# Kernel optimization log

Hardware: AMD Instinct MI355X
Metric: run time of the kernel (lower is better)

Reference implementation:

```python
import jax, jax.numpy as jnp
from jax import lax
import numpy as np

NUM_Q, DIM_S, SIZE_M = 13523, 128, 64
B, T = 64, 200

def setup_inputs() -> dict:
    key = jax.random.key(0)
    ks = jax.random.split(key, 16)
    def kn(k, shape, fan_in):
        # kaiming_normal_ (fan_in, relu gain sqrt(2))
        return jax.random.normal(k, shape, jnp.float32) * np.sqrt(2.0 / fan_in)
    return {
        "q": jax.random.randint(ks[0], (B, T), 0, NUM_Q),
        "r": jax.random.randint(ks[1], (B, T), 0, 2),
        "k_emb": jax.random.normal(ks[2], (NUM_Q, DIM_S), jnp.float32),
        "v_emb": jax.random.normal(ks[3], (2 * NUM_Q, DIM_S), jnp.float32),
        "Mk": kn(ks[4], (SIZE_M, DIM_S), DIM_S),
        "Mv0": kn(ks[5], (SIZE_M, DIM_S), DIM_S),
        "f_W": jax.random.normal(ks[6], (DIM_S, 2 * DIM_S), jnp.float32) / np.sqrt(2 * DIM_S),
        "f_b": jnp.zeros((DIM_S,), jnp.float32),
        "p_W": jax.random.normal(ks[7], (1, DIM_S), jnp.float32) / np.sqrt(DIM_S),
        "p_b": jnp.zeros((1,), jnp.float32),
        "e_W": jax.random.normal(ks[8], (DIM_S, DIM_S), jnp.float32) / np.sqrt(DIM_S),
        "e_b": jnp.zeros((DIM_S,), jnp.float32),
        "a_W": jax.random.normal(ks[9], (DIM_S, DIM_S), jnp.float32) / np.sqrt(DIM_S),
        "a_b": jnp.zeros((DIM_S,), jnp.float32),
    }

def reference(q, r, k_emb, v_emb, Mk, Mv0, f_W, f_b, p_W, p_b, e_W, e_b, a_W, a_b):
    num_q = k_emb.shape[0]
    x = q + num_q * r                       # [B,T]
    k = k_emb[q]                            # [B,T,D]
    v = v_emb[x]                            # [B,T,D]
    w = jax.nn.softmax(jnp.einsum('btd,md->btm', k, Mk), axis=-1)  # [B,T,M]
    e = jax.nn.sigmoid(v @ e_W.T + e_b)     # [B,T,D]
    a = jnp.tanh(v @ a_W.T + a_b)           # [B,T,D]
    batch = q.shape[0]
    Mv_init = jnp.broadcast_to(Mv0, (batch,) + Mv0.shape)  # [B,M,D]

    def step(Mvt, inp):
        wt, et, at = inp  # [B,M],[B,D],[B,D]
        we = wt[:, :, None]  # [B,M,1]
        Mvt = Mvt * (1.0 - we * et[:, None, :]) + we * at[:, None, :]
        return Mvt, Mvt

    _, Mv_seq = lax.scan(step, Mv_init,
                         (w.transpose(1, 0, 2), e.transpose(1, 0, 2), a.transpose(1, 0, 2)))
    # Mv: [B, T+1, M, D], index t holds memory BEFORE write at step t
    Mv = jnp.concatenate([Mv_init[None], Mv_seq], axis=0).transpose(1, 0, 2, 3)
    read = jnp.einsum('btm,btmd->btd', w, Mv[:, :-1])  # read pre-update memory
    f = jnp.tanh(jnp.concatenate([read, k], axis=-1) @ f_W.T + f_b)
    p = jax.nn.sigmoid(f @ p_W.T + p_b).squeeze(-1)    # [B,T]
    return p, Mv
```

## Files before the change

### kernel.cpp

```cpp
#include <hip/hip_runtime.h>
#include <cstdint>
#include <cstddef>

#define B_   64
#define T_   200
#define NQ_  13523
#define NTOK (B_*T_)

#define O_MKT  0
#define O_EWT  8192
#define O_AWT  24576
#define O_FWT  40960
#define O_W    73728
#define O_EV   892928
#define O_AV   2531328
#define O_KF   4169728
#define O_PART 5808128

#define TOKA 32
#define LSTR 36

typedef float f4v __attribute__((ext_vector_type(4)));

__device__ __forceinline__ float sigmoidf_(float x){
  return __fdividef(1.f, 1.f + __expf(-x));
}
__device__ __forceinline__ float tanhf_(float x){
  float ax = fabsf(x);
  float e  = __expf(-2.f*ax);
  float t  = __fdividef(1.f - e, 1.f + e);
  return copysignf(t, x);
}

__device__ __forceinline__ void nt_store4(const float4& v, float* p){
  f4v t; t.x = v.x; t.y = v.y; t.z = v.z; t.w = v.w;
  __builtin_nontemporal_store(t, (f4v*)p);
}

__global__ __launch_bounds__(256) void k_prep(const float* __restrict__ Mk,
    const float* __restrict__ eW, const float* __restrict__ aW,
    const float* __restrict__ fW, float* __restrict__ ws)
{
  int i = blockIdx.x*256 + threadIdx.x;
  if (i < 8192){  int j = i>>6, m = i&63;  ws[O_MKT+i] = Mk[m*128 + j]; }
  if (i < 16384){ int j = i>>7, d = i&127; ws[O_EWT+i] = eW[d*128 + j];
                                           ws[O_AWT+i] = aW[d*128 + j]; }
  if (i < 32768){ int c = i>>7, d = i&127; ws[O_FWT+i] = fW[d*256 + c]; }
}

__global__ __launch_bounds__(256) void k_embed(const int* __restrict__ q,
    const int* __restrict__ r, const float* __restrict__ kE,
    const float* __restrict__ vE, const float* __restrict__ eb,
    const float* __restrict__ ab, float* __restrict__ ws)
{
  __shared__ float Kt[128*LSTR];
  __shared__ float Vt[128*LSTR];
  __shared__ int qx[2*TOKA];
  const int tid = threadIdx.x;
  const int it0 = blockIdx.x * TOKA;

  if (tid < TOKA){
    int qq = q[it0+tid];
    qx[tid]      = qq;
    qx[TOKA+tid] = qq + NQ_*r[it0+tid];
  }
  __syncthreads();

  {
    const int j  = tid & 127;
    const int wg = tid >> 7;
    #pragma unroll
    for (int rr=0; rr<4; ++rr){
      const int i0 = rr*8 + wg*4;
      float4 kv, vv;
      kv.x = kE[(size_t)qx[i0+0]*128 + j];
      kv.y = kE[(size_t)qx[i0+1]*128 + j];
      kv.z = kE[(size_t)qx[i0+2]*128 + j];
      kv.w = kE[(size_t)qx[i0+3]*128 + j];
      vv.x = vE[(size_t)qx[TOKA+i0+0]*128 + j];
      vv.y = vE[(size_t)qx[TOKA+i0+1]*128 + j];
      vv.z = vE[(size_t)qx[TOKA+i0+2]*128 + j];
      vv.w = vE[(size_t)qx[TOKA+i0+3]*128 + j];
      *(float4*)&Kt[j*LSTR + i0] = kv;
      *(float4*)&Vt[j*LSTR + i0] = vv;
    }
  }
  __syncthreads();

  const int lane = tid & 63;
  const int wv   = tid >> 6;

  {
    float acc[8] = {0,0,0,0,0,0,0,0};
    #pragma unroll 4
    for (int j=0;j<128;++j){
      float mk  = ws[O_MKT + j*64 + lane];
      float4 k0 = *(const float4*)&Kt[j*LSTR + wv*8];
      float4 k1 = *(const float4*)&Kt[j*LSTR + wv*8 + 4];
      acc[0] = fmaf(k0.x, mk, acc[0]);
      acc[1] = fmaf(k0.y, mk, acc[1]);
      acc[2] = fmaf(k0.z, mk, acc[2]);
      acc[3] = fmaf(k0.w, mk, acc[3]);
      acc[4] = fmaf(k1.x, mk, acc[4]);
      acc[5] = fmaf(k1.y, mk, acc[5]);
      acc[6] = fmaf(k1.z, mk, acc[6]);
      acc[7] = fmaf(k1.w, mk, acc[7]);
    }
    #pragma unroll
    for (int ii=0;ii<8;++ii){
      float x = acc[ii];
      float mx = x;
      #pragma unroll
      for (int off=32; off>0; off>>=1) mx = fmaxf(mx, __shfl_xor(mx, off));
      float ex = __expf(x - mx);
      float sm = ex;
      #pragma unroll
      for (int off=32; off>0; off>>=1) sm += __shfl_xor(sm, off);
      ws[O_W + (size_t)(it0 + wv*8 + ii)*64 + lane] = __fdividef(ex, sm);
    }
  }

  {
    const int d0 = lane, d1 = lane + 64;
    float aE0[8]={0},aE1[8]={0},aA0[8]={0},aA1[8]={0},aK0[8]={0},aK1[8]={0};
    #pragma unroll 2
    for (int j=0;j<128;++j){
      float we0 = ws[O_EWT + j*128 + d0];
      float we1 = ws[O_EWT + j*128 + d1];
      float wa0 = ws[O_AWT + j*128 + d0];
      float wa1 = ws[O_AWT + j*128 + d1];
      float wf0 = ws[O_FWT + (128+j)*128 + d0];
      float wf1 = ws[O_FWT + (128+j)*128 + d1];
      float4 v0 = *(const float4*)&Vt[j*LSTR + wv*8];
      float4 v1 = *(const float4*)&Vt[j*LSTR + wv*8 + 4];
      float4 k0 = *(const float4*)&Kt[j*LSTR + wv*8];
      float4 k1 = *(const float4*)&Kt[j*LSTR + wv*8 + 4];
      float vv[8] = {v0.x,v0.y,v0.z,v0.w,v1.x,v1.y,v1.z,v1.w};
      float kk[8] = {k0.x,k0.y,k0.z,k0.w,k1.x,k1.y,k1.z,k1.w};
      #pragma unroll
      for (int ii=0;ii<8;++ii){
        aE0[ii] = fmaf(vv[ii], we0, aE0[ii]);
        aE1[ii] = fmaf(vv[ii], we1, aE1[ii]);
        aA0[ii] = fmaf(vv[ii], wa0, aA0[ii]);
        aA1[ii] = fmaf(vv[ii], wa1, aA1[ii]);
        aK0[ii] = fmaf(kk[ii], wf0, aK0[ii]);
        aK1[ii] = fmaf(kk[ii], wf1, aK1[ii]);
      }
    }
    const float eb0 = eb[d0], eb1 = eb[d1];
    const float ab0 = ab[d0], ab1 = ab[d1];
    #pragma unroll
    for (int ii=0;ii<8;++ii){
      size_t it = (size_t)(it0 + wv*8 + ii);
      ws[O_EV + it*128 + d0] = sigmoidf_(aE0[ii] + eb0);
      ws[O_EV + it*128 + d1] = sigmoidf_(aE1[ii] + eb1);
      ws[O_AV + it*128 + d0] = tanhf_(aA0[ii] + ab0);
      ws[O_AV + it*128 + d1] = tanhf_(aA1[ii] + ab1);
      ws[O_KF + it*128 + d0] = aK0[ii];
      ws[O_KF + it*128 + d1] = aK1[ii];
    }
  }
}

__global__ __launch_bounds__(256) void k_scan(const float* __restrict__ Mv0,
    float* __restrict__ ws, float* __restrict__ out)
{
  const int tid = threadIdx.x;
  const int b   = blockIdx.x >> 2;
  const int c   = blockIdx.x & 3;
  const int mgr = tid & 7;
  const int dq  = tid >> 3;
  const int m0  = c*16 + mgr*2;
  const int d0  = dq*4;

  float* mv = out + NTOK + (size_t)b*201*64*128;

  float4 s0 = *(const float4*)&Mv0[(size_t)(m0+0)*128 + d0];
  float4 s1 = *(const float4*)&Mv0[(size_t)(m0+1)*128 + d0];
  nt_store4(s0, &mv[(size_t)(m0+0)*128 + d0]);
  nt_store4(s1, &mv[(size_t)(m0+1)*128 + d0]);

  const float* wp = ws + O_W  + (size_t)b*T_*64  + m0;
  const float* ep = ws + O_EV + (size_t)b*T_*128 + d0;
  const float* ap = ws + O_AV + (size_t)b*T_*128 + d0;
  float* pp = ws + O_PART + (size_t)c*NTOK*128 + (size_t)b*T_*128 + d0;

  float2 wA = *(const float2*)(wp);
  float4 eA = *(const float4*)(ep);
  float4 aA = *(const float4*)(ap);
  float2 wB = *(const float2*)(wp + 64);
  float4 eB = *(const float4*)(ep + 128);
  float4 aB = *(const float4*)(ap + 128);

  for (int t=0; t<T_; ++t){
    const int tn = (t+2 < T_) ? t+2 : T_-1;
    float2 wC = *(const float2*)(wp + (size_t)tn*64);
    float4 eC = *(const float4*)(ep + (size_t)tn*128);
    float4 aC = *(const float4*)(ap + (size_t)tn*128);

    float4 r;
    r.x = fmaf(wA.x, s0.x, wA.y*s1.x);
    r.y = fmaf(wA.x, s0.y, wA.y*s1.y);
    r.z = fmaf(wA.x, s0.z, wA.y*s1.z);
    r.w = fmaf(wA.x, s0.w, wA.y*s1.w);
    #pragma unroll
    for (int off=1; off<8; off<<=1){
      r.x += __shfl_xor(r.x, off);
      r.y += __shfl_xor(r.y, off);
      r.z += __shfl_xor(r.z, off);
      r.w += __shfl_xor(r.w, off);
    }
    if (mgr == 0) *(float4*)&pp[(size_t)t*128] = r;

    float4 u0, u1;
    u0.x = fmaf(-eA.x, s0.x, aA.x);  s0.x = fmaf(wA.x, u0.x, s0.x);
    u0.y = fmaf(-eA.y, s0.y, aA.y);  s0.y = fmaf(wA.x, u0.y, s0.y);
    u0.z = fmaf(-eA.z, s0.z, aA.z);  s0.z = fmaf(wA.x, u0.z, s0.z);
    u0.w = fmaf(-eA.w, s0.w, aA.w);  s0.w = fmaf(wA.x, u0.w, s0.w);
    u1.x = fmaf(-eA.x, s1.x, aA.x);  s1.x = fmaf(wA.y, u1.x, s1.x);
    u1.y = fmaf(-eA.y, s1.y, aA.y);  s1.y = fmaf(wA.y, u1.y, s1.y);
    u1.z = fmaf(-eA.z, s1.z, aA.z);  s1.z = fmaf(wA.y, u1.z, s1.z);
    u1.w = fmaf(-eA.w, s1.w, aA.w);  s1.w = fmaf(wA.y, u1.w, s1.w);

    float* mvt = mv + (size_t)(t+1)*64*128;
    nt_store4(s0, &mvt[(size_t)(m0+0)*128 + d0]);
    nt_store4(s1, &mvt[(size_t)(m0+1)*128 + d0]);

    wA = wB; eA = eB; aA = aB;
    wB = wC; eB = eC; aB = aC;
  }
}

__global__ __launch_bounds__(256) void k_out(const float* __restrict__ ws,
    const float* __restrict__ fb, const float* __restrict__ pW,
    const float* __restrict__ pb, float* __restrict__ out)
{
  __shared__ float Rt[128*LSTR];
  const int tid = threadIdx.x;
  const int it0 = blockIdx.x * TOKA;
  {
    const int j  = tid & 127;
    const int wg = tid >> 7;
    const float* P = ws + O_PART;
    #pragma unroll
    for (int rr=0; rr<4; ++rr){
      const int i0 = rr*8 + wg*4;
      float v4[4];
      #pragma unroll
      for (int ii=0;ii<4;++ii){
        size_t base = (size_t)(it0+i0+ii)*128 + j;
        v4[ii] = P[base] + P[(size_t)NTOK*128 + base]
               + P[2*(size_t)NTOK*128 + base] + P[3*(size_t)NTOK*128 + base];
      }
      *(float4*)&Rt[j*LSTR + i0] = make_float4(v4[0],v4[1],v4[2],v4[3]);
    }
  }
  __syncthreads();
  const int lane = tid & 63, wv = tid >> 6;
  const int d0 = lane, d1 = lane + 64;
  float a0[8]={0,0,0,0,0,0,0,0}, a1[8]={0,0,0,0,0,0,0,0};
  #pragma unroll 2
  for (int j=0;j<128;++j){
    float w0 = ws[O_FWT + j*128 + d0];
    float w1 = ws[O_FWT + j*128 + d1];
    float4 r0 = *(const float4*)&Rt[j*LSTR + wv*8];
    float4 r1 = *(const float4*)&Rt[j*LSTR + wv*8 + 4];
    float rv[8] = {r0.x,r0.y,r0.z,r0.w,r1.x,r1.y,r1.z,r1.w};
    #pragma unroll
    for (int ii=0;ii<8;++ii){
      a0[ii] = fmaf(rv[ii], w0, a0[ii]);
      a1[ii] = fmaf(rv[ii], w1, a1[ii]);
    }
  }
  const float fb0 = fb[d0], fb1 = fb[d1];
  const float pw0 = pW[d0], pw1 = pW[d1];
  #pragma unroll
  for (int ii=0;ii<8;++ii){
    size_t it = (size_t)(it0 + wv*8 + ii);
    float f0 = tanhf_(a0[ii] + ws[O_KF + it*128 + d0] + fb0);
    float f1 = tanhf_(a1[ii] + ws[O_KF + it*128 + d1] + fb1);
    float part = fmaf(f0, pw0, f1*pw1);
    #pragma unroll
    for (int off=32; off>0; off>>=1) part += __shfl_xor(part, off);
    if (lane == 0) out[it] = sigmoidf_(part + pb[0]);
  }
}

extern "C" void kernel_launch(void* const* d_in, const int* in_sizes, int n_in,
                              void* d_out, int out_size, void* d_ws, size_t ws_size,
                              hipStream_t stream)
{
  const int*   q   = (const int*)d_in[0];
  const int*   r   = (const int*)d_in[1];
  const float* kE  = (const float*)d_in[2];
  const float* vE  = (const float*)d_in[3];
  const float* Mk  = (const float*)d_in[4];
  const float* Mv0 = (const float*)d_in[5];
  const float* fW  = (const float*)d_in[6];
  const float* fb  = (const float*)d_in[7];
  const float* pW  = (const float*)d_in[8];
  const float* pb  = (const float*)d_in[9];
  const float* eW  = (const float*)d_in[10];
  const float* eb  = (const float*)d_in[11];
  const float* aW  = (const float*)d_in[12];
  const float* ab  = (const float*)d_in[13];
  float* out = (float*)d_out;
  float* ws  = (float*)d_ws;

  k_prep <<<128, 256, 0, stream>>>(Mk, eW, aW, fW, ws);
  k_embed<<<NTOK/TOKA, 256, 0, stream>>>(q, r, kE, vE, eb, ab, ws);
  k_scan <<<256, 256, 0, stream>>>(Mv0, ws, out);
  k_out  <<<NTOK/TOKA, 256, 0, stream>>>(ws, fb, pW, pb, out);
}
```

Before: 528.0 us.

## Fuse embed and scan kernels with per-tile flags so scan overlaps embedding

Merges the embedding/projection kernel and the recurrent scan kernel into one launch. The first 400 blocks compute embeddings and publish per-tile ready flags with release atomics, and the trailing 256 scan blocks spin on the flags for their batch's tiles before starting. This lets the scan for early batches overlap with embedding of later tiles and removes one kernel boundary. It relies on blocks being dispatched in index order, otherwise spinning scan blocks could deadlock, and it adds polling overhead.

Result: slower. 710.5 us (+34.5%).

```diff
diff --git a/kernel.cpp b/kernel.cpp
--- a/kernel.cpp
+++ b/kernel.cpp
@@ -6,6 +6,7 @@
 #define T_   200
 #define NQ_  13523
 #define NTOK (B_*T_)
+#define NTILE (NTOK/32)
 
 #define O_MKT  0
 #define O_EWT  8192
@@ -22,6 +23,8 @@
 
 typedef float f4v __attribute__((ext_vector_type(4)));
 
+__device__ int g_flg[NTILE];
+
 __device__ __forceinline__ float sigmoidf_(float x){
   return __fdividef(1.f, 1.f + __expf(-x));
 }
@@ -42,192 +45,209 @@
     const float* __restrict__ fW, float* __restrict__ ws)
 {
   int i = blockIdx.x*256 + threadIdx.x;
+  if (i < NTILE) g_flg[i] = 0;
   if (i < 8192){  int j = i>>6, m = i&63;  ws[O_MKT+i] = Mk[m*128 + j]; }
   if (i < 16384){ int j = i>>7, d = i&127; ws[O_EWT+i] = eW[d*128 + j];
                                            ws[O_AWT+i] = aW[d*128 + j]; }
   if (i < 32768){ int c = i>>7, d = i&127; ws[O_FWT+i] = fW[d*256 + c]; }
 }
 
-__global__ __launch_bounds__(256) void k_embed(const int* __restrict__ q,
+__global__ __launch_bounds__(256) void k_fused(const int* __restrict__ q,
     const int* __restrict__ r, const float* __restrict__ kE,
     const float* __restrict__ vE, const float* __restrict__ eb,
-    const float* __restrict__ ab, float* __restrict__ ws)
+    const float* __restrict__ ab, const float* __restrict__ Mv0,
+    float* __restrict__ ws, float* __restrict__ out)
 {
   __shared__ float Kt[128*LSTR];
   __shared__ float Vt[128*LSTR];
   __shared__ int qx[2*TOKA];
   const int tid = threadIdx.x;
-  const int it0 = blockIdx.x * TOKA;
-
-  if (tid < TOKA){
-    int qq = q[it0+tid];
-    qx[tid]      = qq;
-    qx[TOKA+tid] = qq + NQ_*r[it0+tid];
-  }
-  __syncthreads();
-
-  {
-    const int j  = tid & 127;
-    const int wg = tid >> 7;
-    #pragma unroll
-    for (int rr=0; rr<4; ++rr){
-      const int i0 = rr*8 + wg*4;
-      float4 kv, vv;
-      kv.x = kE[(size_t)qx[i0+0]*128 + j];
-      kv.y = kE[(size_t)qx[i0+1]*128 + j];
-      kv.z = kE[(size_t)qx[i0+2]*128 + j];
-      kv.w = kE[(size_t)qx[i0+3]*128 + j];
-      vv.x = vE[(size_t)qx[TOKA+i0+0]*128 + j];
-      vv.y = vE[(size_t)qx[TOKA+i0+1]*128 + j];
-      vv.z = vE[(size_t)qx[TOKA+i0+2]*128 + j];
-      vv.w = vE[(size_t)qx[TOKA+i0+3]*128 + j];
-      *(float4*)&Kt[j*LSTR + i0] = kv;
-      *(float4*)&Vt[j*LSTR + i0] = vv;
-    }
-  }
-  __syncthreads();
-
-  const int lane = tid & 63;
-  const int wv   = tid >> 6;
-
-  {
-    float acc[8] = {0,0,0,0,0,0,0,0};
-    #pragma unroll 4
-    for (int j=0;j<128;++j){
-      float mk  = ws[O_MKT + j*64 + lane];
-      float4 k0 = *(const float4*)&Kt[j*LSTR + wv*8];
-      float4 k1 = *(const float4*)&Kt[j*LSTR + wv*8 + 4];
-      acc[0] = fmaf(k0.x, mk, acc[0]);
-      acc[1] = fmaf(k0.y, mk, acc[1]);
-      acc[2] = fmaf(k0.z, mk, acc[2]);
-      acc[3] = fmaf(k0.w, mk, acc[3]);
-      acc[4] = fmaf(k1.x, mk, acc[4]);
-      acc[5] = fmaf(k1.y, mk, acc[5]);
-      acc[6] = fmaf(k1.z, mk, acc[6]);
-      acc[7] = fmaf(k1.w, mk, acc[7]);
-    }
-    #pragma unroll
-    for (int ii=0;ii<8;++ii){
-      float x = acc[ii];
-      float mx = x;
-      #pragma unroll
-      for (int off=32; off>0; off>>=1) mx = fmaxf(mx, __shfl_xor(mx, off));
-      float ex = __expf(x - mx);
-      float sm = ex;
-      #pragma unroll
-      for (int off=32; off>0; off>>=1) sm += __shfl_xor(sm, off);
-      ws[O_W + (size_t)(it0 + wv*8 + ii)*64 + lane] = __fdividef(ex, sm);
-    }
-  }
-
-  {
-    const int d0 = lane, d1 = lane + 64;
-    float aE0[8]={0},aE1[8]={0},aA0[8]={0},aA1[8]={0},aK0[8]={0},aK1[8]={0};
-    #pragma unroll 2
-    for (int j=0;j<128;++j){
-      float we0 = ws[O_EWT + j*128 + d0];
-      float we1 = ws[O_EWT + j*128 + d1];
-      float wa0 = ws[O_AWT + j*128 + d0];
-      float wa1 = ws[O_AWT + j*128 + d1];
-      float wf0 = ws[O_FWT + (128+j)*128 + d0];
-      float wf1 = ws[O_FWT + (128+j)*128 + d1];
-      float4 v0 = *(const float4*)&Vt[j*LSTR + wv*8];
-      float4 v1 = *(const float4*)&Vt[j*LSTR + wv*8 + 4];
-      float4 k0 = *(const float4*)&Kt[j*LSTR + wv*8];
-      float4 k1 = *(const float4*)&Kt[j*LSTR + wv*8 + 4];
-      float vv[8] = {v0.x,v0.y,v0.z,v0.w,v1.x,v1.y,v1.z,v1.w};
-      float kk[8] = {k0.x,k0.y,k0.z,k0.w,k1.x,k1.y,k1.z,k1.w};
+
+  if (blockIdx.x < NTILE){
+    const int it0 = blockIdx.x * TOKA;
+
+    if (tid < TOKA){
+      int qq = q[it0+tid];
+      qx[tid]      = qq;
+      qx[TOKA+tid] = qq + NQ_*r[it0+tid];
+    }
+    __syncthreads();
+
+    {
+      const int j  = tid & 127;
+      const int wg = tid >> 7;
+      #pragma unroll
+      for (int rr=0; rr<4; ++rr){
+        const int i0 = rr*8 + wg*4;
+        float4 kv, vv;
+        kv.x = kE[(size_t)qx[i0+0]*128 + j];
+        kv.y = kE[(size_t)qx[i0+1]*128 + j];
+        kv.z = kE[(size_t)qx[i0+2]*128 + j];
+        kv.w = kE[(size_t)qx[i0+3]*128 + j];
+        vv.x = vE[(size_t)qx[TOKA+i0+0]*128 + j];
+        vv.y = vE[(size_t)qx[TOKA+i0+1]*128 + j];
+        vv.z = vE[(size_t)qx[TOKA+i0+2]*128 + j];
+        vv.w = vE[(size_t)qx[TOKA+i0+3]*128 + j];
+        *(float4*)&Kt[j*LSTR + i0] = kv;
+        *(float4*)&Vt[j*LSTR + i0] = vv;
+      }
+    }
+    __syncthreads();
+
+    const int lane = tid & 63;
+    const int wv   = tid >> 6;
+
+    {
+      float acc[8] = {0,0,0,0,0,0,0,0};
+      #pragma unroll 4
+      for (int j=0;j<128;++j){
+        float mk  = ws[O_MKT + j*64 + lane];
+        float4 k0 = *(const float4*)&Kt[j*LSTR + wv*8];
+        float4 k1 = *(const float4*)&Kt[j*LSTR + wv*8 + 4];
+        acc[0] = fmaf(k0.x, mk, acc[0]);
+        acc[1] = fmaf(k0.y, mk, acc[1]);
+        acc[2] = fmaf(k0.z, mk, acc[2]);
+        acc[3] = fmaf(k0.w, mk, acc[3]);
+        acc[4] = fmaf(k1.x, mk, acc[4]);
+        acc[5] = fmaf(k1.y, mk, acc[5]);
+        acc[6] = fmaf(k1.z, mk, acc[6]);
+        acc[7] = fmaf(k1.w, mk, acc[7]);
+      }
       #pragma unroll
       for (int ii=0;ii<8;++ii){
-        aE0[ii] = fmaf(vv[ii], we0, aE0[ii]);
-        aE1[ii] = fmaf(vv[ii], we1, aE1[ii]);
-        aA0[ii] = fmaf(vv[ii], wa0, aA0[ii]);
-        aA1[ii] = fmaf(vv[ii], wa1, aA1[ii]);
-        aK0[ii] = fmaf(kk[ii], wf0, aK0[ii]);
-        aK1[ii] = fmaf(kk[ii], wf1, aK1[ii]);
-      }
-    }
-    const float eb0 = eb[d0], eb1 = eb[d1];
-    const float ab0 = ab[d0], ab1 = ab[d1];
-    #pragma unroll
-    for (int ii=0;ii<8;++ii){
-      size_t it = (size_t)(it0 + wv*8 + ii);
-      ws[O_EV + it*128 + d0] = sigmoidf_(aE0[ii] + eb0);
-      ws[O_EV + it*128 + d1] = sigmoidf_(aE1[ii] + eb1);
-      ws[O_AV + it*128 + d0] = tanhf_(aA0[ii] + ab0);
-      ws[O_AV + it*128 + d1] = tanhf_(aA1[ii] + ab1);
-      ws[O_KF + it*128 + d0] = aK0[ii];
-      ws[O_KF + it*128 + d1] = aK1[ii];
-    }
-  }
-}
-
-__global__ __launch_bounds__(256) void k_scan(const float* __restrict__ Mv0,
-    float* __restrict__ ws, float* __restrict__ out)
-{
-  const int tid = threadIdx.x;
-  const int b   = blockIdx.x >> 2;
-  const int c   = blockIdx.x & 3;
-  const int mgr = tid & 7;
-  const int dq  = tid >> 3;
-  const int m0  = c*16 + mgr*2;
-  const int d0  = dq*4;
-
-  float* mv = out + NTOK + (size_t)b*201*64*128;
-
-  float4 s0 = *(const float4*)&Mv0[(size_t)(m0+0)*128 + d0];
-  float4 s1 = *(const float4*)&Mv0[(size_t)(m0+1)*128 + d0];
-  nt_store4(s0, &mv[(size_t)(m0+0)*128 + d0]);
-  nt_store4(s1, &mv[(size_t)(m0+1)*128 + d0]);
-
-  const float* wp = ws + O_W  + (size_t)b*T_*64  + m0;
-  const float* ep = ws + O_EV + (size_t)b*T_*128 + d0;
-  const float* ap = ws + O_AV + (size_t)b*T_*128 + d0;
-  float* pp = ws + O_PART + (size_t)c*NTOK*128 + (size_t)b*T_*128 + d0;
-
-  float2 wA = *(const float2*)(wp);
-  float4 eA = *(const float4*)(ep);
-  float4 aA = *(const float4*)(ap);
-  float2 wB = *(const float2*)(wp + 64);
-  float4 eB = *(const float4*)(ep + 128);
-  float4 aB = *(const float4*)(ap + 128);
-
-  for (int t=0; t<T_; ++t){
-    const int tn = (t+2 < T_) ? t+2 : T_-1;
-    float2 wC = *(const float2*)(wp + (size_t)tn*64);
-    float4 eC = *(const float4*)(ep + (size_t)tn*128);
-    float4 aC = *(const float4*)(ap + (size_t)tn*128);
-
-    float4 r;
-    r.x = fmaf(wA.x, s0.x, wA.y*s1.x);
-    r.y = fmaf(wA.x, s0.y, wA.y*s1.y);
-    r.z = fmaf(wA.x, s0.z, wA.y*s1.z);
-    r.w = fmaf(wA.x, s0.w, wA.y*s1.w);
-    #pragma unroll
-    for (int off=1; off<8; off<<=1){
-      r.x += __shfl_xor(r.x, off);
-      r.y += __shfl_xor(r.y, off);
-      r.z += __shfl_xor(r.z, off);
-      r.w += __shfl_xor(r.w, off);
-    }
-    if (mgr == 0) *(float4*)&pp[(size_t)t*128] = r;
-
-    float4 u0, u1;
-    u0.x = fmaf(-eA.x, s0.x, aA.x);  s0.x = fmaf(wA.x, u0.x, s0.x);
-    u0.y = fmaf(-eA.y, s0.y, aA.y);  s0.y = fmaf(wA.x, u0.y, s0.y);
-    u0.z = fmaf(-eA.z, s0.z, aA.z);  s0.z = fmaf(wA.x, u0.z, s0.z);
-    u0.w = fmaf(-eA.w, s0.w, aA.w);  s0.w = fmaf(wA.x, u0.w, s0.w);
-    u1.x = fmaf(-eA.x, s1.x, aA.x);  s1.x = fmaf(wA.y, u1.x, s1.x);
-    u1.y = fmaf(-eA.y, s1.y, aA.y);  s1.y = fmaf(wA.y, u1.y, s1.y);
-    u1.z = fmaf(-eA.z, s1.z, aA.z);  s1.z = fmaf(wA.y, u1.z, s1.z);
-    u1.w = fmaf(-eA.w, s1.w, aA.w);  s1.w = fmaf(wA.y, u1.w, s1.w);
-
-    float* mvt = mv + (size_t)(t+1)*64*128;
-    nt_store4(s0, &mvt[(size_t)(m0+0)*128 + d0]);
-    nt_store4(s1, &mvt[(size_t)(m0+1)*128 + d0]);
-
-    wA = wB; eA = eB; aA = aB;
-    wB = wC; eB = eC; aB = aC;
+        float x = acc[ii];
+        float mx = x;
+        #pragma unroll
+        for (int off=32; off>0; off>>=1) mx = fmaxf(mx, __shfl_xor(mx, off));
+        float ex = __expf(x - mx);
+        float sm = ex;
+        #pragma unroll
+        for (int off=32; off>0; off>>=1) sm += __shfl_xor(sm, off);
+        ws[O_W + (size_t)(it0 + wv*8 + ii)*64 + lane] = __fdividef(ex, sm);
+      }
+    }
+
+    {
+      const int d0 = lane, d1 = lane + 64;
+      float aE0[8]={0},aE1[8]={0},aA0[8]={0},aA1[8]={0},aK0[8]={0},aK1[8]={0};
+      #pragma unroll 2
+      for (int j=0;j<128;++j){
+        float we0 = ws[O_EWT + j*128 + d0];
+        float we1 = ws[O_EWT + j*128 + d1];
+        float wa0 = ws[O_AWT + j*128 + d0];
+        float wa1 = ws[O_AWT + j*128 + d1];
+        float wf0 = ws[O_FWT + (128+j)*128 + d0];
+        float wf1 = ws[O_FWT + (128+j)*128 + d1];
+        float4 v0 = *(const float4*)&Vt[j*LSTR + wv*8];
+        float4 v1 = *(const float4*)&Vt[j*LSTR + wv*8 + 4];
+        float4 k0 = *(const float4*)&Kt[j*LSTR + wv*8];
+        float4 k1 = *(const float4*)&Kt[j*LSTR + wv*8 + 4];
+        float vv[8] = {v0.x,v0.y,v0.z,v0.w,v1.x,v1.y,v1.z,v1.w};
+        float kk[8] = {k0.x,k0.y,k0.z,k0.w,k1.x,k1.y,k1.z,k1.w};
+        #pragma unroll
+        for (int ii=0;ii<8;++ii){
+          aE0[ii] = fmaf(vv[ii], we0, aE0[ii]);
+          aE1[ii] = fmaf(vv[ii], we1, aE1[ii]);
+          aA0[ii] = fmaf(vv[ii], wa0, aA0[ii]);
+          aA1[ii] = fmaf(vv[ii], wa1, aA1[ii]);
+          aK0[ii] = fmaf(kk[ii], wf0, aK0[ii]);
+          aK1[ii] = fmaf(kk[ii], wf1, aK1[ii]);
+        }
+      }
+      const float eb0 = eb[d0], eb1 = eb[d1];
+      const float ab0 = ab[d0], ab1 = ab[d1];
+      #pragma unroll
+      for (int ii=0;ii<8;++ii){
+        size_t it = (size_t)(it0 + wv*8 + ii);
+        ws[O_EV + it*128 + d0] = sigmoidf_(aE0[ii] + eb0);
+        ws[O_EV + it*128 + d1] = sigmoidf_(aE1[ii] + eb1);
+        ws[O_AV + it*128 + d0] = tanhf_(aA0[ii] + ab0);
+        ws[O_AV + it*128 + d1] = tanhf_(aA1[ii] + ab1);
+        ws[O_KF + it*128 + d0] = aK0[ii];
+        ws[O_KF + it*128 + d1] = aK1[ii];
+      }
+    }
+
+    __threadfence();
+    __syncthreads();
+    if (tid == 0)
+      __hip_atomic_store(&g_flg[blockIdx.x], 1, __ATOMIC_RELEASE,
+                         __HIP_MEMORY_SCOPE_AGENT);
+  } else {
+    const int sb  = blockIdx.x - NTILE;
+    const int b   = sb >> 2;
+    const int c   = sb & 3;
+    const int mgr = tid & 7;
+    const int dq  = tid >> 3;
+    const int m0  = c*16 + mgr*2;
+    const int d0  = dq*4;
+
+    if (tid == 0){
+      const int t0 = (200*b)/32, t1 = (200*b+199)/32;
+      for (int i=t0; i<=t1; ++i){
+        while (__hip_atomic_load(&g_flg[i], __ATOMIC_ACQUIRE,
+                                 __HIP_MEMORY_SCOPE_AGENT) == 0)
+          __builtin_amdgcn_s_sleep(32);
+      }
+    }
+    __syncthreads();
+
+    float* mv = out + NTOK + (size_t)b*201*64*128;
+
+    float4 s0 = *(const float4*)&Mv0[(size_t)(m0+0)*128 + d0];
+    float4 s1 = *(const float4*)&Mv0[(size_t)(m0+1)*128 + d0];
+    nt_store4(s0, &mv[(size_t)(m0+0)*128 + d0]);
+    nt_store4(s1, &mv[(size_t)(m0+1)*128 + d0]);
+
+    const float* wp = ws + O_W  + (size_t)b*T_*64  + m0;
+    const float* ep = ws + O_EV + (size_t)b*T_*128 + d0;
+    const float* ap = ws + O_AV + (size_t)b*T_*128 + d0;
+    float* pp = ws + O_PART + (size_t)c*NTOK*128 + (size_t)b*T_*128 + d0;
+
+    float2 wA = *(const float2*)(wp);
+    float4 eA = *(const float4*)(ep);
+    float4 aA = *(const float4*)(ap);
+    float2 wB = *(const float2*)(wp + 64);
+    float4 eB = *(const float4*)(ep + 128);
+    float4 aB = *(const float4*)(ap + 128);
+
+    for (int t=0; t<T_; ++t){
+      const int tn = (t+2 < T_) ? t+2 : T_-1;
+      float2 wC = *(const float2*)(wp + (size_t)tn*64);
+      float4 eC = *(const float4*)(ep + (size_t)tn*128);
+      float4 aC = *(const float4*)(ap + (size_t)tn*128);
+
+      float4 rr;
+      rr.x = fmaf(wA.x, s0.x, wA.y*s1.x);
+      rr.y = fmaf(wA.x, s0.y, wA.y*s1.y);
+      rr.z = fmaf(wA.x, s0.z, wA.y*s1.z);
+      rr.w = fmaf(wA.x, s0.w, wA.y*s1.w);
+      #pragma unroll
+      for (int off=1; off<8; off<<=1){
+        rr.x += __shfl_xor(rr.x, off);
+        rr.y += __shfl_xor(rr.y, off);
+        rr.z += __shfl_xor(rr.z, off);
+        rr.w += __shfl_xor(rr.w, off);
+      }
+      if (mgr == 0) *(float4*)&pp[(size_t)t*128] = rr;
+
+      float4 u0, u1;
+      u0.x = fmaf(-eA.x, s0.x, aA.x);  s0.x = fmaf(wA.x, u0.x, s0.x);
+      u0.y = fmaf(-eA.y, s0.y, aA.y);  s0.y = fmaf(wA.x, u0.y, s0.y);
+      u0.z = fmaf(-eA.z, s0.z, aA.z);  s0.z = fmaf(wA.x, u0.z, s0.z);
+      u0.w = fmaf(-eA.w, s0.w, aA.w);  s0.w = fmaf(wA.x, u0.w, s0.w);
+      u1.x = fmaf(-eA.x, s1.x, aA.x);  s1.x = fmaf(wA.y, u1.x, s1.x);
+      u1.y = fmaf(-eA.y, s1.y, aA.y);  s1.y = fmaf(wA.y, u1.y, s1.y);
+      u1.z = fmaf(-eA.z, s1.z, aA.z);  s1.z = fmaf(wA.y, u1.z, s1.z);
+      u1.w = fmaf(-eA.w, s1.w, aA.w);  s1.w = fmaf(wA.y, u1.w, s1.w);
+
+      float* mvt = mv + (size_t)(t+1)*64*128;
+      nt_store4(s0, &mvt[(size_t)(m0+0)*128 + d0]);
+      nt_store4(s1, &mvt[(size_t)(m0+1)*128 + d0]);
+
+      wA = wB; eA = eB; aA = aB;
+      wB = wC; eB = eC; aB = aC;
+    }
   }
 }
 
@@ -308,7 +328,6 @@
   float* ws  = (float*)d_ws;
 
   k_prep <<<128, 256, 0, stream>>>(Mk, eW, aW, fW, ws);
-  k_embed<<<NTOK/TOKA, 256, 0, stream>>>(q, r, kE, vE, eb, ab, ws);
-  k_scan <<<256, 256, 0, stream>>>(Mv0, ws, out);
+  k_fused<<<NTILE + 256, 256, 0, stream>>>(q, r, kE, vE, eb, ab, Mv0, ws, out);
   k_out  <<<NTOK/TOKA, 256, 0, stream>>>(ws, fb, pW, pb, out);
 }
```
